# Kernel tuning notes

Measured on AMD Instinct MI355X. Metric: run time of the kernel, lower is better.

Reference implementation:

```python
import math
import jax, jax.numpy as jnp
import numpy as np
from jax import lax

WINDOW_SIZE = 11
SIGMA = 1.5
C1 = 0.01 ** 2
C2 = 0.03 ** 2


def _gauss_window(channel, dtype):
    # matches torch gaussian(window_size, 1.5), normalized, expanded to (channel, 1, size)
    x = np.arange(WINDOW_SIZE)
    g = np.exp(-((x - WINDOW_SIZE // 2) ** 2) / (2.0 * SIGMA ** 2))
    g = g / g.sum()
    w = np.broadcast_to(g[None, None, :], (channel, 1, WINDOW_SIZE))
    return jnp.asarray(w, dtype=dtype)


def _dwconv1d(x, w, channel):
    # depthwise conv1d, padding = window_size // 2 (same length output)
    pad = WINDOW_SIZE // 2
    return lax.conv_general_dilated(
        x, w,
        window_strides=(1,),
        padding=[(pad, pad)],
        dimension_numbers=("NCH", "OIH", "NCH"),
        feature_group_count=channel,
    )


def setup_inputs() -> dict:
    key = jax.random.key(0)
    k1, k2 = jax.random.split(key)
    B, C, T = 16, 32, 48000
    pred = jax.random.normal(k1, (B, C, T), dtype=jnp.float32)
    target = jax.random.normal(k2, (B, C, T), dtype=jnp.float32)
    return {"pred": pred, "target": target}


def reference(pred, target):
    channel = pred.shape[1]
    w = _gauss_window(channel, pred.dtype)

    mu1 = _dwconv1d(pred, w, channel)
    mu2 = _dwconv1d(target, w, channel)
    mu1_sq = mu1 * mu1
    mu2_sq = mu2 * mu2
    mu1_mu2 = mu1 * mu2

    sigma1_sq = _dwconv1d(pred * pred, w, channel) - mu1_sq
    sigma2_sq = _dwconv1d(target * target, w, channel) - mu2_sq
    sigma12 = _dwconv1d(pred * target, w, channel) - mu1_mu2

    ssim_map = ((2 * mu1_mu2 + C1) * (2 * sigma12 + C2)) / (
        (mu1_sq + mu2_sq + C1) * (sigma1_sq + sigma2_sq + C2)
    )
    return jnp.mean(1.0 - ssim_map)
```

## Files before the change

### kernel.cpp

```cpp
#include <hip/hip_runtime.h>
#include <math.h>

constexpr int T     = 48000;
constexpr int TPB   = 192;
constexpr int OPT   = 5;
constexpr int TILE  = TPB * OPT;
constexpr int TPR   = T / TILE;
constexpr int HALO  = 8;
constexpr int SSPAN = TILE + 2 * HALO;
constexpr int NF4   = SSPAN / 4;
constexpr float C1f = 0.0001f;
constexpr float C2f = 0.0009f;

struct W11 { float w[11]; };

__global__ __launch_bounds__(TPB) void ssim_main(
    const float* __restrict__ pred, const float* __restrict__ targ,
    float* __restrict__ partial, W11 wts)
{
    __shared__ __align__(16) float su[SSPAN];
    __shared__ __align__(16) float sv[SSPAN];
    __shared__ float wsum[TPB / 64];

    const int row  = blockIdx.x / TPR;
    const int tile = blockIdx.x % TPR;
    const int ts   = tile * TILE;
    const float* pr = pred + (size_t)row * T;
    const float* tr = targ + (size_t)row * T;

    for (int k = threadIdx.x; k < NF4; k += TPB) {
        const int g4 = ts - HALO + 4 * k;
        float4 a = {0.f, 0.f, 0.f, 0.f}, b = {0.f, 0.f, 0.f, 0.f};
        if (g4 >= 0 && g4 < T) {
            a = *reinterpret_cast<const float4*>(pr + g4);
            b = *reinterpret_cast<const float4*>(tr + g4);
        }
        float4 u, v;
        u.x = a.x + b.x; u.y = a.y + b.y; u.z = a.z + b.z; u.w = a.w + b.w;
        v.x = a.x - b.x; v.y = a.y - b.y; v.z = a.z - b.z; v.w = a.w - b.w;
        *reinterpret_cast<float4*>(su + 4 * k) = u;
        *reinterpret_cast<float4*>(sv + 4 * k) = v;
    }
    __syncthreads();

    const int base = OPT * threadIdx.x + (HALO - 5);
    float u[OPT + 10], v[OPT + 10];
    #pragma unroll
    for (int k = 0; k < OPT + 10; k++) { u[k] = su[base + k]; v[k] = sv[base + k]; }
    float uu[OPT + 10], vv[OPT + 10];
    #pragma unroll
    for (int k = 0; k < OPT + 10; k++) { uu[k] = u[k] * u[k]; vv[k] = v[k] * v[k]; }

    float ca[OPT] = {}, cb[OPT] = {}, cc[OPT] = {}, cd[OPT] = {};
    #pragma unroll
    for (int k = 0; k < 11; k++) {
        const float wk = wts.w[k];
        #pragma unroll
        for (int m = 0; m < OPT; m++) {
            ca[m] = fmaf(wk, u[m + k],  ca[m]);
            cb[m] = fmaf(wk, v[m + k],  cb[m]);
            cc[m] = fmaf(wk, uu[m + k], cc[m]);
            cd[m] = fmaf(wk, vv[m + k], cd[m]);
        }
    }

    float loss = 0.f;
    #pragma unroll
    for (int m = 0; m < OPT; m++) {
        const float aa = ca[m] * ca[m], bb = cb[m] * cb[m];
        const float e  = 0.5f * (aa - bb);
        const float f  = 0.5f * (aa + bb);
        const float t2 = 0.5f * (cc[m] - cd[m]);
        const float sP = 0.5f * (cc[m] + cd[m]);
        const float num = (e + C1f) * (t2 - e + C2f);
        const float den = (f + C1f) * (sP - f + C2f);
        loss += 1.f - num * __builtin_amdgcn_rcpf(den);
    }

    #pragma unroll
    for (int off = 32; off; off >>= 1) loss += __shfl_down(loss, off);
    if ((threadIdx.x & 63) == 0) wsum[threadIdx.x >> 6] = loss;
    __syncthreads();
    if (threadIdx.x == 0) {
        float s = 0.f;
        #pragma unroll
        for (int i = 0; i < TPB / 64; i++) s += wsum[i];
        partial[blockIdx.x] = s;
    }
}

__global__ __launch_bounds__(256) void ssim_reduce(
    const float4* __restrict__ partial4, int n4, float* __restrict__ out, float inv_n)
{
    float s = 0.f;
    for (int i = threadIdx.x; i < n4; i += 256) {
        const float4 p = partial4[i];
        s += (p.x + p.y) + (p.z + p.w);
    }
    #pragma unroll
    for (int off = 32; off; off >>= 1) s += __shfl_down(s, off);
    __shared__ float ws[4];
    if ((threadIdx.x & 63) == 0) ws[threadIdx.x >> 6] = s;
    __syncthreads();
    if (threadIdx.x == 0) {
        float t = 0.f;
        #pragma unroll
        for (int i = 0; i < 4; i++) t += ws[i];
        out[0] = t * inv_n;
    }
}

extern "C" void kernel_launch(void* const* d_in, const int* in_sizes, int n_in,
                              void* d_out, int out_size, void* d_ws, size_t ws_size,
                              hipStream_t stream)
{
    const float* pred = (const float*)d_in[0];
    const float* targ = (const float*)d_in[1];
    float* out = (float*)d_out;
    float* partial = (float*)d_ws;

    const int n      = in_sizes[0];
    const int rows   = n / T;
    const int blocks = rows * TPR;

    W11 wts;
    double g[11], s = 0.0;
    for (int i = 0; i < 11; i++) { g[i] = exp(-((i - 5) * (i - 5)) / 4.5); s += g[i]; }
    for (int i = 0; i < 11; i++) wts.w[i] = (float)(g[i] / s);

    hipLaunchKernelGGL(ssim_main, dim3(blocks), dim3(TPB), 0, stream,
                       pred, targ, partial, wts);
    hipLaunchKernelGGL(ssim_reduce, dim3(1), dim3(256), 0, stream,
                       (const float4*)partial, blocks / 4, out, 1.0f / (float)n);
}
```

Baseline: 61.08 us.

## Replace shared-memory tile staging with per-thread overlapping float4 global loads

Each thread now loads its own 20-sample window of pred and target as five float4 reads straight from global memory, and builds the sum/difference values in registers. This removes the LDS staging buffers and the block barrier that sat between the load and the convolution. Outputs per thread drop from 5 to 4, blocks grow to 256 threads, and an occupancy hint is added. The per-element 1 - ssim subtraction moves into a single final 1 - mean in the reduce kernel. In exchange, neighbouring threads re-read overlapping halo data (about 5x load amplification), which relies on L1/L2 hits to avoid extra DRAM traffic.

```diff
diff --git a/kernel.cpp b/kernel.cpp
--- a/kernel.cpp
+++ b/kernel.cpp
@@ -2,54 +2,65 @@
 #include <math.h>
 
 constexpr int T     = 48000;
-constexpr int TPB   = 192;
-constexpr int OPT   = 5;
-constexpr int TILE  = TPB * OPT;
-constexpr int TPR   = T / TILE;
-constexpr int HALO  = 8;
-constexpr int SSPAN = TILE + 2 * HALO;
-constexpr int NF4   = SSPAN / 4;
+constexpr int TPB   = 256;
+constexpr int OPT   = 4;
+constexpr int TPROW = T / OPT;
 constexpr float C1f = 0.0001f;
 constexpr float C2f = 0.0009f;
 
 struct W11 { float w[11]; };
 
-__global__ __launch_bounds__(TPB) void ssim_main(
+#define KEEP4(v) asm("" : "+v"((v).x), "+v"((v).y), "+v"((v).z), "+v"((v).w))
+
+__global__ __launch_bounds__(TPB, 3) void ssim_main(
     const float* __restrict__ pred, const float* __restrict__ targ,
-    float* __restrict__ partial, W11 wts)
+    float* __restrict__ partial, int nthreads, W11 wts)
 {
-    __shared__ __align__(16) float su[SSPAN];
-    __shared__ __align__(16) float sv[SSPAN];
-    __shared__ float wsum[TPB / 64];
-
-    const int row  = blockIdx.x / TPR;
-    const int tile = blockIdx.x % TPR;
-    const int ts   = tile * TILE;
+    const int tid  = blockIdx.x * TPB + (int)threadIdx.x;
+    const bool live = tid < nthreads;
+    const int t0   = live ? tid : 0;
+    const int row  = t0 / TPROW;
+    const int pos  = (t0 - row * TPROW) * OPT;
     const float* pr = pred + (size_t)row * T;
     const float* tr = targ + (size_t)row * T;
+    const int g0 = pos - 8;
 
-    for (int k = threadIdx.x; k < NF4; k += TPB) {
-        const int g4 = ts - HALO + 4 * k;
-        float4 a = {0.f, 0.f, 0.f, 0.f}, b = {0.f, 0.f, 0.f, 0.f};
-        if (g4 >= 0 && g4 < T) {
-            a = *reinterpret_cast<const float4*>(pr + g4);
-            b = *reinterpret_cast<const float4*>(tr + g4);
+    float4 pq[5], tq[5];
+    if (pos >= 8 && pos + 12 <= T) {
+        const float4* P4 = reinterpret_cast<const float4*>(pr + g0);
+        const float4* Q4 = reinterpret_cast<const float4*>(tr + g0);
+        #pragma unroll
+        for (int j = 0; j < 5; j++) { pq[j] = P4[j]; tq[j] = Q4[j]; }
+    } else {
+        #pragma unroll
+        for (int j = 0; j < 5; j++) {
+            const int q = g0 + 4 * j;
+            float4 a = {0.f,0.f,0.f,0.f}, b = {0.f,0.f,0.f,0.f};
+            if (q >= 0 && q + 4 <= T) {
+                a = *reinterpret_cast<const float4*>(pr + q);
+                b = *reinterpret_cast<const float4*>(tr + q);
+            }
+            pq[j] = a; tq[j] = b;
         }
-        float4 u, v;
-        u.x = a.x + b.x; u.y = a.y + b.y; u.z = a.z + b.z; u.w = a.w + b.w;
-        v.x = a.x - b.x; v.y = a.y - b.y; v.z = a.z - b.z; v.w = a.w - b.w;
-        *reinterpret_cast<float4*>(su + 4 * k) = u;
-        *reinterpret_cast<float4*>(sv + 4 * k) = v;
     }
-    __syncthreads();
+    #pragma unroll
+    for (int j = 0; j < 5; j++) { KEEP4(pq[j]); KEEP4(tq[j]); }
 
-    const int base = OPT * threadIdx.x + (HALO - 5);
-    float u[OPT + 10], v[OPT + 10];
+    const float P[20] = {pq[0].x,pq[0].y,pq[0].z,pq[0].w, pq[1].x,pq[1].y,pq[1].z,pq[1].w,
+                         pq[2].x,pq[2].y,pq[2].z,pq[2].w, pq[3].x,pq[3].y,pq[3].z,pq[3].w,
+                         pq[4].x,pq[4].y,pq[4].z,pq[4].w};
+    const float Q[20] = {tq[0].x,tq[0].y,tq[0].z,tq[0].w, tq[1].x,tq[1].y,tq[1].z,tq[1].w,
+                         tq[2].x,tq[2].y,tq[2].z,tq[2].w, tq[3].x,tq[3].y,tq[3].z,tq[3].w,
+                         tq[4].x,tq[4].y,tq[4].z,tq[4].w};
+
+    float U[17], V[17], UU[17], VV[17];
     #pragma unroll
-    for (int k = 0; k < OPT + 10; k++) { u[k] = su[base + k]; v[k] = sv[base + k]; }
-    float uu[OPT + 10], vv[OPT + 10];
-    #pragma unroll
-    for (int k = 0; k < OPT + 10; k++) { uu[k] = u[k] * u[k]; vv[k] = v[k] * v[k]; }
+    for (int i = 3; i <= 16; i++) {
+        U[i] = P[i] + Q[i];
+        V[i] = P[i] - Q[i];
+        UU[i] = U[i] * U[i];
+        VV[i] = V[i] * V[i];
+    }
 
     float ca[OPT] = {}, cb[OPT] = {}, cc[OPT] = {}, cd[OPT] = {};
     #pragma unroll
@@ -57,14 +68,14 @@
         const float wk = wts.w[k];
         #pragma unroll
         for (int m = 0; m < OPT; m++) {
-            ca[m] = fmaf(wk, u[m + k],  ca[m]);
-            cb[m] = fmaf(wk, v[m + k],  cb[m]);
-            cc[m] = fmaf(wk, uu[m + k], cc[m]);
-            cd[m] = fmaf(wk, vv[m + k], cd[m]);
+            ca[m] = fmaf(wk, U[3 + m + k],  ca[m]);
+            cb[m] = fmaf(wk, V[3 + m + k],  cb[m]);
+            cc[m] = fmaf(wk, UU[3 + m + k], cc[m]);
+            cd[m] = fmaf(wk, VV[3 + m + k], cd[m]);
         }
     }
 
-    float loss = 0.f;
+    float qsum = 0.f;
     #pragma unroll
     for (int m = 0; m < OPT; m++) {
         const float aa = ca[m] * ca[m], bb = cb[m] * cb[m];
@@ -74,12 +85,14 @@
         const float sP = 0.5f * (cc[m] + cd[m]);
         const float num = (e + C1f) * (t2 - e + C2f);
         const float den = (f + C1f) * (sP - f + C2f);
-        loss += 1.f - num * __builtin_amdgcn_rcpf(den);
+        qsum += num * __builtin_amdgcn_rcpf(den);
     }
+    qsum = live ? qsum : 0.f;
 
     #pragma unroll
-    for (int off = 32; off; off >>= 1) loss += __shfl_down(loss, off);
-    if ((threadIdx.x & 63) == 0) wsum[threadIdx.x >> 6] = loss;
+    for (int off = 32; off; off >>= 1) qsum += __shfl_down(qsum, off);
+    __shared__ float wsum[TPB / 64];
+    if ((threadIdx.x & 63) == 0) wsum[threadIdx.x >> 6] = qsum;
     __syncthreads();
     if (threadIdx.x == 0) {
         float s = 0.f;
@@ -106,7 +119,7 @@
         float t = 0.f;
         #pragma unroll
         for (int i = 0; i < 4; i++) t += ws[i];
-        out[0] = t * inv_n;
+        out[0] = 1.f - t * inv_n;
     }
 }
 
@@ -119,9 +132,10 @@
     float* out = (float*)d_out;
     float* partial = (float*)d_ws;
 
-    const int n      = in_sizes[0];
-    const int rows   = n / T;
-    const int blocks = rows * TPR;
+    const int n        = in_sizes[0];
+    const int rows     = n / T;
+    const int nthreads = rows * TPROW;
+    const int blocks   = (nthreads + TPB - 1) / TPB;
 
     W11 wts;
     double g[11], s = 0.0;
@@ -129,7 +143,7 @@
     for (int i = 0; i < 11; i++) wts.w[i] = (float)(g[i] / s);
 
     hipLaunchKernelGGL(ssim_main, dim3(blocks), dim3(TPB), 0, stream,
-                       pred, targ, partial, wts);
+                       pred, targ, partial, nthreads, wts);
     hipLaunchKernelGGL(ssim_reduce, dim3(1), dim3(256), 0, stream,
                        (const float4*)partial, blocks / 4, out, 1.0f / (float)n);
 }
```

Measured after the change: 63.25 us. +3.6%, slower.
